# Kernel optimization log

Measured on AMD Instinct MI355X. Metric: run time of the kernel, lower is better.

The kernel has to match this reference:

```python
import jax, jax.numpy as jnp
import numpy as np

B, S, E, D = 256, 256, 2, 128  # batch, seq_len, encoder_dim, decoder_dim


def setup_inputs() -> dict:
    key = jax.random.key(0)
    ks = jax.random.split(key, 9)
    u = lambda k, shape, n: jax.random.uniform(k, shape, jnp.float32, -1.0 / np.sqrt(n), 1.0 / np.sqrt(n))
    return {
        "out_encoder": jax.random.normal(ks[0], (B, S, E), jnp.float32),
        "W1_w": u(ks[1], (S, S), S),            # Linear(seq_len, seq_len)
        "W1_b": u(ks[2], (S,), S),
        "W2_w": u(ks[3], (S, 2 * S), 2 * S),    # Linear(2*seq_len, seq_len)
        "W2_b": u(ks[4], (S,), 2 * S),
        "W_ih": u(ks[5], (4 * D, E), D),        # LSTMCell input weights (i,f,g,o)
        "W_hh": u(ks[6], (4 * D, D), D),
        "b_ih": u(ks[7], (4 * D,), D),
        "b_hh": u(ks[8], (4 * D,), D),
    }


def reference(out_encoder, W1_w, W1_b, W2_w, W2_b, W_ih, W_hh, b_ih, b_hh):
    b, s, e = out_encoder.shape
    d = W_hh.shape[1]
    dt = out_encoder.dtype

    # W_2 term: encoder flattened to [B, 2S]; identical every step, hoist it.
    w2term = out_encoder.reshape(b, s * e) @ W2_w.T + W2_b          # [B, S]
    # W_1 applied to a row of S copies of h_d equals h_d * rowsum(W1) + b.
    w1sum = W1_w.sum(axis=1)                                        # [S]

    def attn(h):  # h: [B, D] -> context [B, E]
        hterm = h[:, :, None] * w1sum[None, None, :] + W1_b         # [B, D, S]
        en = jnp.tanh(w2term[:, None, :] + hterm)                   # [B, D, S]
        alpha = jax.nn.softmax(en, axis=-1).mean(axis=1)            # [B, S] (softmax over seq)
        return jnp.einsum('bs,bse->be', alpha, out_encoder)         # [B, E]

    def lstm_cell(x, h, c):
        gates = x @ W_ih.T + h @ W_hh.T + b_ih + b_hh               # [B, 4D]
        i, f, g, o = jnp.split(gates, 4, axis=-1)
        c = jax.nn.sigmoid(f) * c + jax.nn.sigmoid(i) * jnp.tanh(g)
        h = jax.nn.sigmoid(o) * jnp.tanh(c)
        return h, c

    h0 = jnp.zeros((b, d), dt)
    c0 = jnp.zeros((b, d), dt)

    def step(carry, _):
        h, c = carry
        x = attn(h)
        h, c = lstm_cell(x, h, c)
        return (h, c), h

    _, hs = jax.lax.scan(step, (h0, c0), None, length=s)
    return hs  # [S, B, D]: stacked decoder hidden states (original returns a list of h_t)
```

## Files before the change

kernel.cpp:

```cpp
#include <hip/hip_runtime.h>

#define NB 256
#define NS 256
#define NE 2
#define ND 128
#define NT 512
#define NN 16
#define RING 32
#define SLOT 144
#define SLOTH 160

typedef float vf4 __attribute__((ext_vector_type(4)));
typedef _Float16 f16x8 __attribute__((ext_vector_type(8)));
typedef float f32x4 __attribute__((ext_vector_type(4)));

constexpr float L2E = 1.4426950408889634f;
constexpr float PI_F = 3.14159265358979323846f;

__device__ const float CT[16][16] = {
 {1,0,0,0,0,0,0,0,0,0,0,0,0,0,0,0},
 {0,1,0,0,0,0,0,0,0,0,0,0,0,0,0,0},
 {-1,0,2,0,0,0,0,0,0,0,0,0,0,0,0,0},
 {0,-3,0,4,0,0,0,0,0,0,0,0,0,0,0,0},
 {1,0,-8,0,8,0,0,0,0,0,0,0,0,0,0,0},
 {0,5,0,-20,0,16,0,0,0,0,0,0,0,0,0,0},
 {-1,0,18,0,-48,0,32,0,0,0,0,0,0,0,0,0},
 {0,-7,0,56,0,-112,0,64,0,0,0,0,0,0,0,0},
 {1,0,-32,0,160,0,-256,0,128,0,0,0,0,0,0,0},
 {0,9,0,-120,0,432,0,-576,0,256,0,0,0,0,0},
 {-1,0,50,0,-400,0,1120,0,-1280,0,512,0,0,0,0,0},
 {0,-11,0,220,0,-1232,0,2816,0,-2816,0,1024,0,0,0,0},
 {1,0,-72,0,840,0,-3584,0,6912,0,-6144,0,2048,0,0,0},
 {0,13,0,-364,0,2912,0,-9984,0,16640,0,-13312,0,4096,0,0},
 {-1,0,98,0,-1568,0,9408,0,-26880,0,39424,0,-28672,0,8192,0},
 {0,-15,0,560,0,-6048,0,28800,0,-70400,0,92160,0,-61440,0,16384}};

template <int C>
__device__ __forceinline__ float dppadd(float x) {
    return x + __builtin_bit_cast(float,
        __builtin_amdgcn_update_dpp(0, __builtin_bit_cast(int, x), C, 0xF, 0xF, true));
}
template <int C>
__device__ __forceinline__ float quadbc(float x) {
    return __builtin_bit_cast(float,
        __builtin_amdgcn_update_dpp(0, __builtin_bit_cast(int, x), C, 0xF, 0xF, true));
}
__device__ __forceinline__ float red_quad(float x) {
    x = dppadd<0xB1>(x); x = dppadd<0x4E>(x); return x;
}
__device__ __forceinline__ float red_oct(float x) {
    x = dppadd<0xB1>(x); x = dppadd<0x4E>(x); x = dppadd<0x141>(x); return x;
}
__device__ __forceinline__ float red_wave64(float x) {
    x = dppadd<0xB1>(x); x = dppadd<0x4E>(x); x = dppadd<0x141>(x);
    x = dppadd<0x140>(x); x = dppadd<0x142>(x); x = dppadd<0x143>(x); return x;
}
__device__ __forceinline__ float red_half32(float x) {
    x = dppadd<0xB1>(x); x = dppadd<0x4E>(x); x = dppadd<0x141>(x);
    x = dppadd<0x140>(x); x = dppadd<0x142>(x); return x;
}
__device__ __forceinline__ float red_grp16(float x) {
    x = dppadd<0x141>(x); x = dppadd<0x140>(x);
    x = dppadd<0x142>(x); x = dppadd<0x143>(x); return x;
}

__global__ __launch_bounds__(NT, 2)
void attn_lstm_decoder(const float* __restrict__ enc,
                       const float* __restrict__ W1w,
                       const float* __restrict__ W1b,
                       const float* __restrict__ W2w,
                       const float* __restrict__ W2b,
                       const float* __restrict__ Wih,
                       const float* __restrict__ Whh,
                       const float* __restrict__ bih,
                       const float* __restrict__ bhh,
                       float* __restrict__ out)
{
    const int b    = blockIdx.x;
    const int t    = threadIdx.x;
    const int wave = t >> 6;
    const int lane = t & 63;
    const int g    = t >> 2;
    const int q    = t & 3;
    const bool qb0 = q & 1;
    const bool qb1 = q & 2;
    const int grp  = lane >> 4;
    const int nib  = lane & 15;
    const int half = lane >> 5;
    const int idx  = lane & 31;
    const int jnode = 2 * wave + half;

    __shared__ __align__(16) float    hist[RING * SLOT];
    __shared__ __align__(16) _Float16 hist16[RING * SLOTH];
    __shared__ __align__(16) float xwbuf[2][16];
    __shared__ float A2_l[NS];
    __shared__ float g2_l[NS];
    __shared__ float e0_l[NS];
    __shared__ float e1_l[NS];
    __shared__ float Ml[NN * NN];
    __shared__ float2 Pn[NN];
    __shared__ float2 Vl[NN];
    __shared__ float Pm0[NN], Pm1[NN];

    {
        float v = enc[b * (NS * NE) + t];
        if (t & 1) e1_l[t >> 1] = v; else e0_l[t >> 1] = v;
    }
    if (t < NN * NN) {
        const int mi = t >> 4, mj = t & 15;
        const float w = (mi == 0) ? (1.0f / NN) : (2.0f / NN);
        Ml[t] = w * __cosf((float)(mi * (2 * mj + 1)) * (PI_F / (2 * NN)));
    }
    __syncthreads();

    for (int r = 0; r < 32; ++r) {
        const int s = wave * 32 + r;
        float p = W1w[s * NS + lane]       + W1w[s * NS + lane + 64]
                + W1w[s * NS + lane + 128] + W1w[s * NS + lane + 192];
        p = red_wave64(p);
        if (lane == 63) g2_l[s] = p * (2.0f * L2E);
        float qq = 0.0f;
        #pragma unroll
        for (int kk = 0; kk < 8; ++kk) {
            const int c = lane + kk * 64;
            const float ev = (c & 1) ? e1_l[c >> 1] : e0_l[c >> 1];
            qq = fmaf(ev, W2w[s * (2 * NS) + c], qq);
        }
        qq = red_wave64(qq);
        if (lane == 63) A2_l[s] = (qq + W2b[s] + W1b[s]) * (2.0f * L2E);
    }
    __syncthreads();

    {
        const float y  = __cosf((float)(2 * jnode + 1) * (PI_F / (2 * NN)));
        const float C2 = -2.0f * L2E;
        float l = 0.0f, p0 = 0.0f, p1 = 0.0f;
        #pragma unroll
        for (int k = 0; k < 8; ++k) {
            const int s = k * 32 + idx;
            const float m1 = fmaf(y, g2_l[s], A2_l[s]);
            const float u  = __builtin_amdgcn_exp2f(m1);
            const float rc = __builtin_amdgcn_rcpf(u + 1.0f);
            const float e  = __builtin_amdgcn_exp2f(rc * C2);
            l += e;
            p0 = fmaf(e, e0_l[s], p0);
            p1 = fmaf(e, e1_l[s], p1);
        }
        l = red_half32(l); p0 = red_half32(p0); p1 = red_half32(p1);
        if ((lane & 31) == 31) {
            const float rl = __builtin_amdgcn_rcpf(l);
            Pn[jnode] = make_float2(p0 * rl, p1 * rl);
        }
    }
    __syncthreads();

    if (t < NN) {
        float v0 = 0.0f, v1 = 0.0f;
        #pragma unroll
        for (int j = 0; j < NN; ++j) {
            v0 = fmaf(Ml[t * NN + j], Pn[j].x, v0);
            v1 = fmaf(Ml[t * NN + j], Pn[j].y, v1);
        }
        Vl[t] = make_float2(v0 * (1.0f / ND), v1 * (1.0f / ND));
    }

    f16x8 wf[4][4];
    #pragma unroll
    for (int rt = 0; rt < 4; ++rt) {
        const int row = 128 * rt + 16 * wave + nib;
        #pragma unroll
        for (int kt = 0; kt < 4; ++kt) {
            const vf4 wa = *reinterpret_cast<const vf4*>(Whh + row * ND + 32 * kt + 8 * grp);
            const vf4 wb = *reinterpret_cast<const vf4*>(Whh + row * ND + 32 * kt + 8 * grp + 4);
            f16x8 wv;
            wv[0] = (_Float16)wa.x; wv[1] = (_Float16)wa.y;
            wv[2] = (_Float16)wa.z; wv[3] = (_Float16)wa.w;
            wv[4] = (_Float16)wb.x; wv[5] = (_Float16)wb.y;
            wv[6] = (_Float16)wb.z; wv[7] = (_Float16)wb.w;
            wf[rt][kt] = wv;
        }
    }
    const int rq = 128 * q + g;
    const float wiq0 = Wih[rq * 2 + 0];
    const float wiq1 = Wih[rq * 2 + 1];
    const float bbq  = bih[rq] + bhh[rq];
    const float sA  = (q == 2) ? (2.0f * L2E) : (-L2E);
    const float cA1 = (q == 2) ? -2.0f : 1.0f;
    const float cA0 = (q == 2) ? 1.0f : 0.0f;
    const int bidx = ((((lane & 3) << 4) | (lane >> 2)) << 2);

    if (t < ND) {
        hist[31 * SLOT + 36 * (t >> 5) + (t & 31)] = 0.0f;
        hist16[31 * SLOTH + 40 * (t >> 5) + (t & 31)] = (_Float16)0.0f;
    }
    float h_reg = 0.0f, c_reg = 0.0f;
    __syncthreads();

    if (t < NN) {
        float s0 = 0.0f, s1 = 0.0f;
        #pragma unroll
        for (int k = 0; k < NN; ++k) {
            s0 = fmaf(Vl[k].x, CT[k][t], s0);
            s1 = fmaf(Vl[k].y, CT[k][t], s1);
        }
        Pm0[t] = s0; Pm1[t] = s1;
    }
    __syncthreads();

    float Q0[4], Q1[4];
    #pragma unroll
    for (int i = 0; i < 4; ++i) { Q0[i] = Pm0[4 * i + q]; Q1[i] = Pm1[4 * i + q]; }

    auto phaseG = [&](float h, int pw) {
        const float h2 = h * h;
        const float h3 = h2 * h;
        const float h4 = h2 * h2;
        const float hq = qb1 ? (qb0 ? h3 : h2) : (qb0 ? h : 1.0f);
        float a0 = fmaf(Q0[3], h4, Q0[2]);
        a0 = fmaf(a0, h4, Q0[1]);
        a0 = fmaf(a0, h4, Q0[0]);
        float a1 = fmaf(Q1[3], h4, Q1[2]);
        a1 = fmaf(a1, h4, Q1[1]);
        a1 = fmaf(a1, h4, Q1[0]);
        a0 *= hq;
        a1 *= hq;
        a0 = red_quad(a0);  a1 = red_quad(a1);
        a0 = red_grp16(a0); a1 = red_grp16(a1);
        if (lane == 63) {
            xwbuf[pw][2 * wave + 0] = a0;
            xwbuf[pw][2 * wave + 1] = a1;
        }
    };

    phaseG(0.0f, 0);
    __syncthreads();

    for (int step = 0; step < NS; ++step) {
        const int pr = step & 1;
        const int rs = (step + RING - 1) & (RING - 1);
        const int ws = step & (RING - 1);

        f16x8 af[4];
        const _Float16* hsl = &hist16[rs * SLOTH + 8 * grp];
        #pragma unroll
        for (int kt = 0; kt < 4; ++kt)
            af[kt] = __builtin_bit_cast(f16x8,
                *reinterpret_cast<const int4*>(hsl + 40 * kt));

        float2 xv = *reinterpret_cast<const float2*>(&xwbuf[pr][2 * (lane & 7)]);

        if ((step & 15) == 0 && step > 0) {
            const int sb  = (step - 16) & (RING - 1);
            const int k   = t >> 5;
            const int l32 = t & 31;
            const int w   = 4 * l32;
            const vf4 v = *reinterpret_cast<const vf4*>(
                &hist[(sb + k) * SLOT + 36 * (w >> 5) + (w & 31)]);
            *reinterpret_cast<vf4*>(
                &out[(size_t)(step - 16 + k) * (NB * ND) + b * ND + w]) = v;
        }

        float x0 = red_oct(xv.x);
        float x1 = red_oct(xv.y);

        f32x4 acc[4];
        #pragma unroll
        for (int rt = 0; rt < 4; ++rt) {
            f32x4 a = {0.0f, 0.0f, 0.0f, 0.0f};
            #pragma unroll
            for (int kt = 0; kt < 4; ++kt)
                a = __builtin_amdgcn_mfma_f32_16x16x32_f16(af[kt], wf[rt][kt], a, 0, 0, 0);
            acc[rt] = a;
        }

        const float a01 = (lane & 16) ? acc[1][0] : acc[0][0];
        const float a23 = (lane & 16) ? acc[3][0] : acc[2][0];
        const float av  = (lane & 32) ? a23 : a01;
        const float myg = __builtin_bit_cast(float,
            __builtin_amdgcn_ds_bpermute(bidx, __builtin_bit_cast(int, av)));

        const float gq  = myg + fmaf(x0, wiq0, fmaf(x1, wiq1, bbq));
        const float act = fmaf(cA1,
            __builtin_amdgcn_rcpf(1.0f + __builtin_amdgcn_exp2f(sA * gq)), cA0);
        const float si = quadbc<0x00>(act);
        const float sf = quadbc<0x55>(act);
        const float tg = quadbc<0xAA>(act);
        const float so = quadbc<0xFF>(act);

        c_reg = fmaf(sf, c_reg, si * tg);
        const float tc2 = 1.0f - 2.0f * __builtin_amdgcn_rcpf(
            __builtin_amdgcn_exp2f(2.0f * L2E * c_reg) + 1.0f);
        h_reg = so * tc2;

        if (q == 0) {
            hist[ws * SLOT + 36 * (g >> 5) + (g & 31)] = h_reg;
            hist16[ws * SLOTH + 40 * (g >> 5) + (g & 31)] = (_Float16)h_reg;
        }
        phaseG(h_reg, pr ^ 1);

        __syncthreads();
    }

    {
        const int k   = t >> 5;
        const int l32 = t & 31;
        const int w   = 4 * l32;
        const vf4 v = *reinterpret_cast<const vf4*>(
            &hist[(16 + k) * SLOT + 36 * (w >> 5) + (w & 31)]);
        *reinterpret_cast<vf4*>(
            &out[(size_t)(240 + k) * (NB * ND) + b * ND + w]) = v;
    }
}

extern "C" void kernel_launch(void* const* d_in, const int* in_sizes, int n_in,
                              void* d_out, int out_size, void* d_ws, size_t ws_size,
                              hipStream_t stream) {
    const float* enc = (const float*)d_in[0];
    const float* W1w = (const float*)d_in[1];
    const float* W1b = (const float*)d_in[2];
    const float* W2w = (const float*)d_in[3];
    const float* W2b = (const float*)d_in[4];
    const float* Wih = (const float*)d_in[5];
    const float* Whh = (const float*)d_in[6];
    const float* bih = (const float*)d_in[7];
    const float* bhh = (const float*)d_in[8];
    attn_lstm_decoder<<<NB, NT, 0, stream>>>(enc, W1w, W1b, W2w, W2b,
                                             Wih, Whh, bih, bhh, (float*)d_out);
}
```

Measured before the change: 261.5 us.

## Compute attention context redundantly per wave from fp16 history instead of cross-wave buffer

Each wave now evaluates the degree-15 polynomial approximation of the attention context for all 128 hidden units, reading h pairs from the fp16 history ring and reducing with a full-wave DPP reduction plus readlane. This replaces the per-wave partial sums that were written to a shared double buffer and combined after the barrier. The goal is to shorten the serial per-step dependency chain by dropping the shared-memory round trip. In exchange every wave repeats the full polynomial work, the context is computed from fp16-rounded h, and launch bounds drop to one block per CU, which allows more registers.

```diff
diff --git a/kernel.cpp b/kernel.cpp
--- a/kernel.cpp
+++ b/kernel.cpp
@@ -12,6 +12,7 @@
 
 typedef float vf4 __attribute__((ext_vector_type(4)));
 typedef _Float16 f16x8 __attribute__((ext_vector_type(8)));
+typedef _Float16 f16x2 __attribute__((ext_vector_type(2)));
 typedef float f32x4 __attribute__((ext_vector_type(4)));
 
 constexpr float L2E = 1.4426950408889634f;
@@ -45,12 +46,6 @@
     return __builtin_bit_cast(float,
         __builtin_amdgcn_update_dpp(0, __builtin_bit_cast(int, x), C, 0xF, 0xF, true));
 }
-__device__ __forceinline__ float red_quad(float x) {
-    x = dppadd<0xB1>(x); x = dppadd<0x4E>(x); return x;
-}
-__device__ __forceinline__ float red_oct(float x) {
-    x = dppadd<0xB1>(x); x = dppadd<0x4E>(x); x = dppadd<0x141>(x); return x;
-}
 __device__ __forceinline__ float red_wave64(float x) {
     x = dppadd<0xB1>(x); x = dppadd<0x4E>(x); x = dppadd<0x141>(x);
     x = dppadd<0x140>(x); x = dppadd<0x142>(x); x = dppadd<0x143>(x); return x;
@@ -59,12 +54,8 @@
     x = dppadd<0xB1>(x); x = dppadd<0x4E>(x); x = dppadd<0x141>(x);
     x = dppadd<0x140>(x); x = dppadd<0x142>(x); return x;
 }
-__device__ __forceinline__ float red_grp16(float x) {
-    x = dppadd<0x141>(x); x = dppadd<0x140>(x);
-    x = dppadd<0x142>(x); x = dppadd<0x143>(x); return x;
-}
-
-__global__ __launch_bounds__(NT, 2)
+
+__global__ __launch_bounds__(NT, 1)
 void attn_lstm_decoder(const float* __restrict__ enc,
                        const float* __restrict__ W1w,
                        const float* __restrict__ W1b,
@@ -82,8 +73,6 @@
     const int lane = t & 63;
     const int g    = t >> 2;
     const int q    = t & 3;
-    const bool qb0 = q & 1;
-    const bool qb1 = q & 2;
     const int grp  = lane >> 4;
     const int nib  = lane & 15;
     const int half = lane >> 5;
@@ -92,7 +81,6 @@
 
     __shared__ __align__(16) float    hist[RING * SLOT];
     __shared__ __align__(16) _Float16 hist16[RING * SLOTH];
-    __shared__ __align__(16) float xwbuf[2][16];
     __shared__ float A2_l[NS];
     __shared__ float g2_l[NS];
     __shared__ float e0_l[NS];
@@ -207,36 +195,25 @@
     }
     __syncthreads();
 
-    float Q0[4], Q1[4];
+    float cc0[16], cc1[16];
     #pragma unroll
-    for (int i = 0; i < 4; ++i) { Q0[i] = Pm0[4 * i + q]; Q1[i] = Pm1[4 * i + q]; }
-
-    auto phaseG = [&](float h, int pw) {
+    for (int i = 0; i < 16; ++i) { cc0[i] = Pm0[i]; cc1[i] = Pm1[i]; }
+
+    auto evalG = [&](float h, const float (&C)[16]) -> float {
         const float h2 = h * h;
-        const float h3 = h2 * h;
-        const float h4 = h2 * h2;
-        const float hq = qb1 ? (qb0 ? h3 : h2) : (qb0 ? h : 1.0f);
-        float a0 = fmaf(Q0[3], h4, Q0[2]);
-        a0 = fmaf(a0, h4, Q0[1]);
-        a0 = fmaf(a0, h4, Q0[0]);
-        float a1 = fmaf(Q1[3], h4, Q1[2]);
-        a1 = fmaf(a1, h4, Q1[1]);
-        a1 = fmaf(a1, h4, Q1[0]);
-        a0 *= hq;
-        a1 *= hq;
-        a0 = red_quad(a0);  a1 = red_quad(a1);
-        a0 = red_grp16(a0); a1 = red_grp16(a1);
-        if (lane == 63) {
-            xwbuf[pw][2 * wave + 0] = a0;
-            xwbuf[pw][2 * wave + 1] = a1;
-        }
+        float e = C[14], o = C[15];
+        #pragma unroll
+        for (int k = 12; k >= 0; k -= 2) {
+            e = fmaf(e, h2, C[k]);
+            o = fmaf(o, h2, C[k + 1]);
+        }
+        return fmaf(h, o, e);
     };
 
-    phaseG(0.0f, 0);
-    __syncthreads();
+    const int jpair = 32 * (nib >> 2) + 8 * grp + 2 * (nib & 3);
+    const int jpoff = 40 * (jpair >> 5) + (jpair & 31);
 
     for (int step = 0; step < NS; ++step) {
-        const int pr = step & 1;
         const int rs = (step + RING - 1) & (RING - 1);
         const int ws = step & (RING - 1);
 
@@ -246,8 +223,7 @@
         for (int kt = 0; kt < 4; ++kt)
             af[kt] = __builtin_bit_cast(f16x8,
                 *reinterpret_cast<const int4*>(hsl + 40 * kt));
-
-        float2 xv = *reinterpret_cast<const float2*>(&xwbuf[pr][2 * (lane & 7)]);
+        const f16x2 hp2 = *reinterpret_cast<const f16x2*>(&hist16[rs * SLOTH + jpoff]);
 
         if ((step & 15) == 0 && step > 0) {
             const int sb  = (step - 16) & (RING - 1);
@@ -260,9 +236,6 @@
                 &out[(size_t)(step - 16 + k) * (NB * ND) + b * ND + w]) = v;
         }
 
-        float x0 = red_oct(xv.x);
-        float x1 = red_oct(xv.y);
-
         f32x4 acc[4];
         #pragma unroll
         for (int rt = 0; rt < 4; ++rt) {
@@ -272,6 +245,16 @@
                 a = __builtin_amdgcn_mfma_f32_16x16x32_f16(af[kt], wf[rt][kt], a, 0, 0, 0);
             acc[rt] = a;
         }
+
+        const float ha = (float)hp2[0];
+        const float hc = (float)hp2[1];
+        float p0 = evalG(ha, cc0) + evalG(hc, cc0);
+        float p1 = evalG(ha, cc1) + evalG(hc, cc1);
+        p0 = red_wave64(p0); p1 = red_wave64(p1);
+        const float x0 = __builtin_bit_cast(float,
+            __builtin_amdgcn_readlane(__builtin_bit_cast(int, p0), 63));
+        const float x1 = __builtin_bit_cast(float,
+            __builtin_amdgcn_readlane(__builtin_bit_cast(int, p1), 63));
 
         const float a01 = (lane & 16) ? acc[1][0] : acc[0][0];
         const float a23 = (lane & 16) ? acc[3][0] : acc[2][0];
@@ -296,7 +279,6 @@
             hist[ws * SLOT + 36 * (g >> 5) + (g & 31)] = h_reg;
             hist16[ws * SLOTH + 40 * (g >> 5) + (g & 31)] = (_Float16)h_reg;
         }
-        phaseG(h_reg, pr ^ 1);
 
         __syncthreads();
     }
```

Result: slower. 284.2 us (+8.7%).
